# Kernel tuning notes

Measured on AMD Instinct MI355X. Metric: run time of the kernel, lower is better.

The kernel has to match this reference:

```python
import jax, jax.numpy as jnp
import numpy as np

B, L, HID, H = 2, 384, 512, 8
D = HID // H  # head_dim = 64


def setup_inputs() -> dict:
    key = jax.random.key(0)
    ks = jax.random.split(key, 16)
    s = 0.02
    return {
        "query": jax.random.normal(ks[0], (B, L, HID), jnp.float32),
        "key_": jax.random.normal(ks[1], (B, L, HID), jnp.float32),
        "value": jax.random.normal(ks[2], (B, L, HID), jnp.float32),
        "mask": jnp.ones((B, 1, 1, L), jnp.int32),
        # fc_q/k/v/o: nn.Linear(hid_dim, hid_dim)
        "Wq": jax.random.normal(ks[3], (HID, HID), jnp.float32) * s,
        "bq": jnp.zeros((HID,), jnp.float32),
        "Wk": jax.random.normal(ks[4], (HID, HID), jnp.float32) * s,
        "bk": jnp.zeros((HID,), jnp.float32),
        "Wv": jax.random.normal(ks[5], (HID, HID), jnp.float32) * s,
        "bv": jnp.zeros((HID,), jnp.float32),
        "Wo": jax.random.normal(ks[6], (HID, HID), jnp.float32) * s,
        "bo": jnp.zeros((HID,), jnp.float32),
        # additive-attention score MLP: W1, W2: Linear(D, D); v: Linear(D, 1)
        "W1": jax.random.normal(ks[7], (D, D), jnp.float32) * s,
        "b1": jnp.zeros((D,), jnp.float32),
        "W2": jax.random.normal(ks[8], (D, D), jnp.float32) * s,
        "b2": jnp.zeros((D,), jnp.float32),
        "vw": jax.random.normal(ks[9], (1, D), jnp.float32) * s,
        "vb": jnp.zeros((1,), jnp.float32),
    }


def reference(query, key_, value, mask, Wq, bq, Wk, bk, Wv, bv, Wo, bo,
              W1, b1, W2, b2, vw, vb):
    b = query.shape[0]
    # projections (torch Linear: x @ W.T + b)
    Q = query @ Wq.T + bq
    K = key_ @ Wk.T + bk
    V = value @ Wv.T + bv
    # [b, h, l, d]
    def split_heads(x):
        return x.reshape(b, -1, H, D).transpose(0, 2, 1, 3)
    Q, K, V = split_heads(Q), split_heads(K), split_heads(V)
    # additive (Bahdanau-style) score: v^T tanh(W1 q + W2 k)
    tQ = Q @ W1.T + b1            # [b, h, lq, d]
    tK = K @ W2.T + b2            # [b, h, lk, d]
    e = jnp.tanh(tQ[:, :, :, None, :] + tK[:, :, None, :, :])  # [b,h,lq,lk,d]
    energy = jnp.einsum('bhqkd,d->bhqk', e, vw[0]) + vb[0]      # [b,h,lq,lk]
    energy = jnp.where(mask == 0, jnp.float32(-1e10), energy)
    attention = jax.nn.softmax(energy, axis=-1)
    x = jnp.einsum('bhqk,bhkd->bhqd', attention, V)  # dropout p=0 (eval)
    x = x.transpose(0, 2, 1, 3).reshape(b, -1, HID)
    x = x @ Wo.T + bo
    return x, attention
```

## Files before the change

kernel.cpp:

```cpp
#include <hip/hip_runtime.h>

#define BATCH 2
#define LSEQ 384
#define NHID 512
#define NH 8
#define DH 64
#define BH (BATCH*NH)
#define MROWS (BATCH*NH*LSEQ/NH)
#define XELEMS ((size_t)768 * NHID)
#define TQ 8
#define QTILES (LSEQ/TQ)

typedef unsigned short ushort_t;
typedef __attribute__((ext_vector_type(8))) short bf16x8;
typedef __attribute__((ext_vector_type(4))) float f32x4;

__device__ __forceinline__ float bf2f(ushort_t u) {
    unsigned int v = ((unsigned int)u) << 16;
    return __uint_as_float(v);
}
__device__ __forceinline__ ushort_t f2bf(float f) {
    unsigned int u = __float_as_uint(f);
    unsigned int lsb = (u >> 16) & 1u;
    u += 0x7fffu + lsb;
    return (ushort_t)(u >> 16);
}
__device__ __forceinline__ float ld1(const void* p, size_t i, int f) {
    return f ? ((const float*)p)[i] : bf2f(((const ushort_t*)p)[i]);
}
__device__ __forceinline__ float4 ld4(const void* p, size_t i, int f) {
    if (f) return ((const float4*)p)[i >> 2];
    ushort4 u = ((const ushort4*)p)[i >> 2];
    return make_float4(bf2f(u.x), bf2f(u.y), bf2f(u.z), bf2f(u.w));
}
__device__ __forceinline__ int block_detect(const unsigned int* q, int* cnt) {
    int t = threadIdx.x;
    if (t == 0) *cnt = 0;
    __syncthreads();
    int n = blockDim.x < 256 ? blockDim.x : 256;
    if (t < n) {
        unsigned int elo = (q[t] >> 7) & 0xFFu;
        if (elo >= 100u && elo <= 150u) atomicAdd(cnt, 1);
    }
    __syncthreads();
    return (*cnt * 2 > n) ? 0 : 1;
}
__device__ __forceinline__ uint4 packu4(float4 a, float4 b) {
    uint4 r;
    r.x = (unsigned)f2bf(a.x) | ((unsigned)f2bf(a.y) << 16);
    r.y = (unsigned)f2bf(a.z) | ((unsigned)f2bf(a.w) << 16);
    r.z = (unsigned)f2bf(b.x) | ((unsigned)f2bf(b.y) << 16);
    r.w = (unsigned)f2bf(b.z) | ((unsigned)f2bf(b.w) << 16);
    return r;
}
__device__ __forceinline__ bf16x8 pack_bf8(float4 a, float4 b) {
    bf16x8 r;
    r[0] = (short)f2bf(a.x); r[1] = (short)f2bf(a.y);
    r[2] = (short)f2bf(a.z); r[3] = (short)f2bf(a.w);
    r[4] = (short)f2bf(b.x); r[5] = (short)f2bf(b.y);
    r[6] = (short)f2bf(b.z); r[7] = (short)f2bf(b.w);
    return r;
}

#define OFF_ETQ   16
#define OFF_ETKT  (16 + 393216)
#define OFF_VH    (16 + 2*393216)
#define OFF_XH    (16 + 3*393216)

#define LDSTR 72

__global__ __launch_bounds__(128) void gemm_qkv(
    const void* qp, const void* kp, const void* vp,
    const void* Wqp, const void* Wkp, const void* Wvp,
    const void* W1p, const void* W2p,
    const void* bqp, const void* bkp, const void* b1p, const void* b2p,
    const void* bvp, float* __restrict__ ws)
{
    __shared__ int s_cnt;
    __shared__ ushort_t smA[32 * LDSTR];
    __shared__ ushort_t smB[64 * LDSTR];
    __shared__ float biasF[64];
    const int f = block_detect((const unsigned int*)qp, &s_cnt);

    const int mode = blockIdx.z;
    const void* A = (mode == 0) ? qp : (mode == 1) ? kp : vp;
    const void* W = (mode == 0) ? Wqp : (mode == 1) ? Wkp : Wvp;
    const void* W1x = (mode == 1) ? W2p : W1p;

    const int h    = blockIdx.x;
    const int col0 = h * 64;
    const int row0 = blockIdx.y * 32;
    const int t = threadIdx.x;
    const int w = t >> 6, l16 = t & 15, quad = (t & 63) >> 4;

    if (t < 64) {
        if (mode == 2) {
            biasF[t] = ld1(bvp, col0 + t, f);
        } else {
            const void* b1x = (mode == 1) ? b2p : b1p;
            const void* bx  = (mode == 1) ? bkp : bqp;
            float s = ld1(b1x, t, f);
            for (int j = 0; j < 64; j++)
                s = fmaf(ld1(W1x, (size_t)t * 64 + j, f), ld1(bx, h * 64 + j, f), s);
            biasF[t] = s;
        }
    }

    const int arow = t >> 2, acol = (t & 3) * 16;
    const int brow = t >> 1, bcol = (t & 1) * 32;

    const size_t abase = (size_t)(row0 + arow) * 512 + acol;
    const size_t bbase = (size_t)(col0 + brow) * 512 + bcol;

    float4 a4[4], b4[8];
    #pragma unroll
    for (int i = 0; i < 4; i++) a4[i] = ld4(A, abase + i * 4, f);
    #pragma unroll
    for (int i = 0; i < 8; i++) b4[i] = ld4(W, bbase + i * 4, f);

    f32x4 acc[4];
    #pragma unroll
    for (int nt = 0; nt < 4; nt++) acc[nt] = (f32x4){0.f, 0.f, 0.f, 0.f};

    for (int k0 = 0; k0 < 512; k0 += 64) {
        __syncthreads();
        *reinterpret_cast<uint4*>(&smA[arow * LDSTR + acol])     = packu4(a4[0], a4[1]);
        *reinterpret_cast<uint4*>(&smA[arow * LDSTR + acol + 8]) = packu4(a4[2], a4[3]);
        *reinterpret_cast<uint4*>(&smB[brow * LDSTR + bcol])      = packu4(b4[0], b4[1]);
        *reinterpret_cast<uint4*>(&smB[brow * LDSTR + bcol + 8])  = packu4(b4[2], b4[3]);
        *reinterpret_cast<uint4*>(&smB[brow * LDSTR + bcol + 16]) = packu4(b4[4], b4[5]);
        *reinterpret_cast<uint4*>(&smB[brow * LDSTR + bcol + 24]) = packu4(b4[6], b4[7]);
        __syncthreads();
        if (k0 + 64 < 512) {
            #pragma unroll
            for (int i = 0; i < 4; i++) a4[i] = ld4(A, abase + k0 + 64 + i * 4, f);
            #pragma unroll
            for (int i = 0; i < 8; i++) b4[i] = ld4(W, bbase + k0 + 64 + i * 4, f);
        }
        #pragma unroll
        for (int kk = 0; kk < 2; kk++) {
            bf16x8 af = *reinterpret_cast<const bf16x8*>(
                &smA[(w * 16 + l16) * LDSTR + kk * 32 + quad * 8]);
            #pragma unroll
            for (int nt = 0; nt < 4; nt++) {
                bf16x8 bfr = *reinterpret_cast<const bf16x8*>(
                    &smB[(nt * 16 + l16) * LDSTR + kk * 32 + quad * 8]);
                acc[nt] = __builtin_amdgcn_mfma_f32_16x16x32_bf16(af, bfr, acc[nt], 0, 0, 0);
            }
        }
    }

    const int b  = (row0 >= LSEQ) ? 1 : 0;
    const int lbase = row0 - b * LSEQ + w * 16;
    const int bh = b * NH + h;

    if (mode == 2) {
        float* Out = ws + OFF_VH;
        #pragma unroll
        for (int nt = 0; nt < 4; nt++) {
            int d = l16 + nt * 16;
            #pragma unroll
            for (int r = 0; r < 4; r++) {
                int l = lbase + quad * 4 + r;
                Out[(size_t)(bh * LSEQ + l) * 64 + d] = acc[nt][r] + biasF[d];
            }
        }
    } else {
        #pragma unroll
        for (int nt = 0; nt < 4; nt++)
            #pragma unroll
            for (int r = 0; r < 4; r++)
                smA[(w * 16 + quad * 4 + r) * LDSTR + l16 + nt * 16] =
                    f2bf(acc[nt][r]);
        f32x4 acc2[4];
        #pragma unroll
        for (int nt = 0; nt < 4; nt++) acc2[nt] = (f32x4){0.f, 0.f, 0.f, 0.f};
        #pragma unroll
        for (int kk = 0; kk < 2; kk++) {
            bf16x8 af2 = *reinterpret_cast<const bf16x8*>(
                &smA[(w * 16 + l16) * LDSTR + kk * 32 + quad * 8]);
            #pragma unroll
            for (int nt = 0; nt < 4; nt++) {
                int od = nt * 16 + l16, j0 = kk * 32 + quad * 8;
                float4 wa = ld4(W1x, (size_t)od * 64 + j0, f);
                float4 wb = ld4(W1x, (size_t)od * 64 + j0 + 4, f);
                bf16x8 bfw = pack_bf8(wa, wb);
                acc2[nt] = __builtin_amdgcn_mfma_f32_16x16x32_bf16(af2, bfw, acc2[nt], 0, 0, 0);
            }
        }
        if (mode == 0) {
            float* Out = ws + OFF_ETQ;
            #pragma unroll
            for (int nt = 0; nt < 4; nt++) {
                int d = l16 + nt * 16;
                #pragma unroll
                for (int r = 0; r < 4; r++) {
                    int l = lbase + quad * 4 + r;
                    Out[(size_t)(bh * LSEQ + l) * 64 + d] =
                        __expf(2.f * (acc2[nt][r] + biasF[d]));
                }
            }
        } else {
            float* Out = ws + OFF_ETKT;
            #pragma unroll
            for (int nt = 0; nt < 4; nt++) {
                int d = l16 + nt * 16;
                float4 o;
                o.x = __expf(2.f * (acc2[nt][0] + biasF[d]));
                o.y = __expf(2.f * (acc2[nt][1] + biasF[d]));
                o.z = __expf(2.f * (acc2[nt][2] + biasF[d]));
                o.w = __expf(2.f * (acc2[nt][3] + biasF[d]));
                *reinterpret_cast<float4*>(
                    &Out[(size_t)(bh * 64 + d) * LSEQ + lbase + quad * 4]) = o;
            }
        }
    }
}

__global__ __launch_bounds__(384, 6) void attn_kernel(
    const void* qp, const void* vwp, const void* vbp,
    const float* __restrict__ ws_in, float* __restrict__ ws,
    const int* __restrict__ mask, void* __restrict__ dout)
{
    __shared__ int s_cnt;
    const int f = block_detect((const unsigned int*)qp, &s_cnt);

    const float* Etq = ws_in + OFF_ETQ;
    const float* Etk = ws_in + OFF_ETKT;
    const float* Vh  = ws_in + OFF_VH;
    float* Xh = ws + OFF_XH;

    const int bid = blockIdx.x;
    const int qt = bid % QTILES;
    const int bh = bid / QTILES;
    const int q0 = qt * TQ;
    const int b  = bh >> 3;
    const int h  = bh & 7;
    const int t  = threadIdx.x;
    const int wave = t >> 6;

    __shared__ __align__(16) float etq8[64][TQ];
    __shared__ float vws[64];
    __shared__ float ps[TQ][LSEQ];
    __shared__ float red[6][TQ][16][4];
    __shared__ float rmax[TQ][6];
    __shared__ float rsum[TQ][6];
    __shared__ float s_vb;

    for (int i = t; i < TQ * 64; i += 384) {
        int qi = i >> 6, d = i & 63;
        etq8[d][qi] = Etq[(size_t)(bh * LSEQ + q0 + qi) * 64 + d];
    }
    if (t < 64) {
        float v = ld1(vwp, t, f);
        vws[t] = v;
        #pragma unroll
        for (int off = 32; off > 0; off >>= 1) v += __shfl_xor(v, off, 64);
        if (t == 0) s_vb = ld1(vbp, 0, f) + v;
    }
    const int mok = mask[b * LSEQ + t];
    __syncthreads();
    const float vbSum = s_vb;

    float e2[TQ] = {0.f, 0.f, 0.f, 0.f, 0.f, 0.f, 0.f, 0.f};
    const float* ekp = Etk + (size_t)bh * 64 * LSEQ + t;
    #pragma unroll 4
    for (int d = 0; d < 64; d++) {
        float ekv = ekp[(size_t)d * LSEQ];
        float4 eqA = *reinterpret_cast<const float4*>(&etq8[d][0]);
        float4 eqB = *reinterpret_cast<const float4*>(&etq8[d][4]);
        float wv = vws[d];
        e2[0] = fmaf(wv, __builtin_amdgcn_rcpf(fmaf(eqA.x, ekv, 1.0f)), e2[0]);
        e2[1] = fmaf(wv, __builtin_amdgcn_rcpf(fmaf(eqA.y, ekv, 1.0f)), e2[1]);
        e2[2] = fmaf(wv, __builtin_amdgcn_rcpf(fmaf(eqA.z, ekv, 1.0f)), e2[2]);
        e2[3] = fmaf(wv, __builtin_amdgcn_rcpf(fmaf(eqA.w, ekv, 1.0f)), e2[3]);
        e2[4] = fmaf(wv, __builtin_amdgcn_rcpf(fmaf(eqB.x, ekv, 1.0f)), e2[4]);
        e2[5] = fmaf(wv, __builtin_amdgcn_rcpf(fmaf(eqB.y, ekv, 1.0f)), e2[5]);
        e2[6] = fmaf(wv, __builtin_amdgcn_rcpf(fmaf(eqB.z, ekv, 1.0f)), e2[6]);
        e2[7] = fmaf(wv, __builtin_amdgcn_rcpf(fmaf(eqB.w, ekv, 1.0f)), e2[7]);
    }
    float en[TQ];
    #pragma unroll
    for (int qi = 0; qi < TQ; qi++) {
        en[qi] = fmaf(-2.0f, e2[qi], vbSum);
        if (mok == 0) en[qi] = -1e10f;
    }

    #pragma unroll
    for (int qi = 0; qi < TQ; qi++) {
        float m = en[qi];
        #pragma unroll
        for (int off = 32; off > 0; off >>= 1) m = fmaxf(m, __shfl_xor(m, off, 64));
        if ((t & 63) == 0) rmax[qi][wave] = m;
    }
    __syncthreads();
    float p[TQ];
    #pragma unroll
    for (int qi = 0; qi < TQ; qi++) {
        float gm = fmaxf(fmaxf(fmaxf(rmax[qi][0], rmax[qi][1]),
                               fmaxf(rmax[qi][2], rmax[qi][3])),
                         fmaxf(rmax[qi][4], rmax[qi][5]));
        p[qi] = __expf(en[qi] - gm);
        float s = p[qi];
        #pragma unroll
        for (int off = 32; off > 0; off >>= 1) s += __shfl_xor(s, off, 64);
        if ((t & 63) == 0) rsum[qi][wave] = s;
    }
    __syncthreads();
    #pragma unroll
    for (int qi = 0; qi < TQ; qi++) {
        float gs = rsum[qi][0] + rsum[qi][1] + rsum[qi][2] +
                   rsum[qi][3] + rsum[qi][4] + rsum[qi][5];
        p[qi] *= 1.0f / gs;
        ps[qi][t] = p[qi];
        size_t aidx = XELEMS + (size_t)(bh * LSEQ + q0 + qi) * LSEQ + t;
        if (f) ((float*)dout)[aidx] = p[qi];
        else   ((ushort_t*)dout)[aidx] = f2bf(p[qi]);
    }
    __syncthreads();

    const int dq = t & 15;
    const int ksub = t >> 4;
    const float* vb4 = Vh + (size_t)bh * LSEQ * 64 + dq * 4;
    float4 acc[TQ];
    #pragma unroll
    for (int qi = 0; qi < TQ; qi++) acc[qi] = make_float4(0.f, 0.f, 0.f, 0.f);
    for (int kk = ksub; kk < LSEQ; kk += 24) {
        float4 v4 = *reinterpret_cast<const float4*>(vb4 + (size_t)kk * 64);
        #pragma unroll
        for (int qi = 0; qi < TQ; qi++) {
            float pq = ps[qi][kk];
            acc[qi].x = fmaf(pq, v4.x, acc[qi].x);
            acc[qi].y = fmaf(pq, v4.y, acc[qi].y);
            acc[qi].z = fmaf(pq, v4.z, acc[qi].z);
            acc[qi].w = fmaf(pq, v4.w, acc[qi].w);
        }
    }
    #pragma unroll
    for (int qi = 0; qi < TQ; qi++) {
        #pragma unroll
        for (int off = 16; off <= 32; off <<= 1) {
            acc[qi].x += __shfl_xor(acc[qi].x, off, 64);
            acc[qi].y += __shfl_xor(acc[qi].y, off, 64);
            acc[qi].z += __shfl_xor(acc[qi].z, off, 64);
            acc[qi].w += __shfl_xor(acc[qi].w, off, 64);
        }
    }
    if ((t & 63) < 16) {
        #pragma unroll
        for (int qi = 0; qi < TQ; qi++) {
            red[wave][qi][dq][0] = acc[qi].x;
            red[wave][qi][dq][1] = acc[qi].y;
            red[wave][qi][dq][2] = acc[qi].z;
            red[wave][qi][dq][3] = acc[qi].w;
        }
    }
    __syncthreads();
    if (t < 256) {
        int d = t & 63;
        #pragma unroll
        for (int half = 0; half < 2; half++) {
            int qi = (t >> 6) + half * 4;
            float sx = 0.f;
            #pragma unroll
            for (int w = 0; w < 6; w++) sx += red[w][qi][d >> 2][d & 3];
            Xh[((size_t)(b * LSEQ + q0 + qi) * NH + h) * 64 + d] = sx;
        }
    }
}

__global__ __launch_bounds__(128) void gemm_out(
    const void* qp, const void* Wop, const void* bop,
    const float* __restrict__ ws_in, void* __restrict__ dout)
{
    __shared__ int s_cnt;
    __shared__ ushort_t smA[32 * LDSTR];
    __shared__ ushort_t smB[64 * LDSTR];
    __shared__ float biasF[64];
    const int f = block_detect((const unsigned int*)qp, &s_cnt);

    const float* Xh = ws_in + OFF_XH;
    const int col0 = blockIdx.x * 64;
    const int row0 = blockIdx.y * 32;
    const int t = threadIdx.x;
    const int w = t >> 6, l16 = t & 15, quad = (t & 63) >> 4;

    if (t < 64) biasF[t] = ld1(bop, col0 + t, f);

    const int arow = t >> 2, acol = (t & 3) * 16;
    const int brow = t >> 1, bcol = (t & 1) * 32;
    const float* Ab = Xh + (size_t)(row0 + arow) * 512 + acol;
    const size_t bbase = (size_t)(col0 + brow) * 512 + bcol;

    float4 a4[4], b4[8];
    #pragma unroll
    for (int i = 0; i < 4; i++) a4[i] = *reinterpret_cast<const float4*>(Ab + i * 4);
    #pragma unroll
    for (int i = 0; i < 8; i++) b4[i] = ld4(Wop, bbase + i * 4, f);

    f32x4 acc[4];
    #pragma unroll
    for (int nt = 0; nt < 4; nt++) acc[nt] = (f32x4){0.f, 0.f, 0.f, 0.f};

    for (int k0 = 0; k0 < 512; k0 += 64) {
        __syncthreads();
        *reinterpret_cast<uint4*>(&smA[arow * LDSTR + acol])     = packu4(a4[0], a4[1]);
        *reinterpret_cast<uint4*>(&smA[arow * LDSTR + acol + 8]) = packu4(a4[2], a4[3]);
        *reinterpret_cast<uint4*>(&smB[brow * LDSTR + bcol])      = packu4(b4[0], b4[1]);
        *reinterpret_cast<uint4*>(&smB[brow * LDSTR + bcol + 8])  = packu4(b4[2], b4[3]);
        *reinterpret_cast<uint4*>(&smB[brow * LDSTR + bcol + 16]) = packu4(b4[4], b4[5]);
        *reinterpret_cast<uint4*>(&smB[brow * LDSTR + bcol + 24]) = packu4(b4[6], b4[7]);
        __syncthreads();
        if (k0 + 64 < 512) {
            #pragma unroll
            for (int i = 0; i < 4; i++)
                a4[i] = *reinterpret_cast<const float4*>(Ab + k0 + 64 + i * 4);
            #pragma unroll
            for (int i = 0; i < 8; i++) b4[i] = ld4(Wop, bbase + k0 + 64 + i * 4, f);
        }
        #pragma unroll
        for (int kk = 0; kk < 2; kk++) {
            bf16x8 af = *reinterpret_cast<const bf16x8*>(
                &smA[(w * 16 + l16) * LDSTR + kk * 32 + quad * 8]);
            #pragma unroll
            for (int nt = 0; nt < 4; nt++) {
                bf16x8 bfr = *reinterpret_cast<const bf16x8*>(
                    &smB[(nt * 16 + l16) * LDSTR + kk * 32 + quad * 8]);
                acc[nt] = __builtin_amdgcn_mfma_f32_16x16x32_bf16(af, bfr, acc[nt], 0, 0, 0);
            }
        }
    }

    #pragma unroll
    for (int nt = 0; nt < 4; nt++) {
        int n = col0 + l16 + nt * 16;
        float bi = biasF[l16 + nt * 16];
        #pragma unroll
        for (int r = 0; r < 4; r++) {
            int m = row0 + w * 16 + quad * 4 + r;
            float c = acc[nt][r] + bi;
            size_t idx = (size_t)m * 512 + n;
            if (f) ((float*)dout)[idx] = c;
            else   ((ushort_t*)dout)[idx] = f2bf(c);
        }
    }
}

extern "C" void kernel_launch(void* const* d_in, const int* in_sizes, int n_in,
                              void* d_out, int out_size, void* d_ws, size_t ws_size,
                              hipStream_t stream)
{
    const void* qp = d_in[0];
    const void* kp = d_in[1];
    const void* vp = d_in[2];
    const int* mask = (const int*)d_in[3];
    const void* Wqp = d_in[4];  const void* bqp = d_in[5];
    const void* Wkp = d_in[6];  const void* bkp = d_in[7];
    const void* Wvp = d_in[8];  const void* bvp = d_in[9];
    const void* Wop = d_in[10]; const void* bop = d_in[11];
    const void* W1p = d_in[12]; const void* b1p = d_in[13];
    const void* W2p = d_in[14]; const void* b2p = d_in[15];
    const void* vwp = d_in[16]; const void* vbp = d_in[17];

    float* ws = (float*)d_ws;

    gemm_qkv<<<dim3(8, 24, 3), 128, 0, stream>>>(qp, kp, vp, Wqp, Wkp, Wvp,
                                                 W1p, W2p, bqp, bkp, b1p, b2p,
                                                 bvp, ws);
    attn_kernel<<<BH * QTILES, 384, 0, stream>>>(qp, vwp, vbp, ws, ws, mask, d_out);
    gemm_out<<<dim3(8, 24, 1), 128, 0, stream>>>(qp, Wop, bop, ws, d_out);
}
```

Before: 169.0 us.

## Split-K the QKV and output GEMMs and drop the softmax max pass

The QKV projection GEMM is split into two K halves and the output GEMM into four. Each split writes fp32 partials to workspace, and new finalize/out_reduce kernels add them, apply the bias, exp and transpose, and write the bf16 or fp32 result. The goal is more blocks to fill the GPU than the earlier 192/576-block grids provided. This costs two extra launches and extra workspace traffic. Separately, the attention kernel drops the row-max reduction and its syncthreads before exp. That relies on bounded energies and risks overflow, and with a -1e10 mask an all-masked row gives a zero sum.

```diff
diff --git a/kernel.cpp b/kernel.cpp
--- a/kernel.cpp
+++ b/kernel.cpp
@@ -6,7 +6,6 @@
 #define NH 8
 #define DH 64
 #define BH (BATCH*NH)
-#define MROWS (BATCH*NH*LSEQ/NH)
 #define XELEMS ((size_t)768 * NHID)
 #define TQ 8
 #define QTILES (LSEQ/TQ)
@@ -62,10 +61,14 @@
     return r;
 }
 
-#define OFF_ETQ   16
-#define OFF_ETKT  (16 + 393216)
-#define OFF_VH    (16 + 2*393216)
-#define OFF_XH    (16 + 3*393216)
+#define OFF_P     16
+#define PSTRIDE   393216
+#define OFF_BQE   2359312
+#define OFF_BKE   2359824
+#define OFF_ETQ   2360336
+#define OFF_ETKT  2753552
+#define OFF_VH    3146768
+#define OFF_XH    3539984
 
 #define LDSTR 72
 
@@ -74,18 +77,20 @@
     const void* Wqp, const void* Wkp, const void* Wvp,
     const void* W1p, const void* W2p,
     const void* bqp, const void* bkp, const void* b1p, const void* b2p,
-    const void* bvp, float* __restrict__ ws)
+    float* __restrict__ ws)
 {
     __shared__ int s_cnt;
     __shared__ ushort_t smA[32 * LDSTR];
     __shared__ ushort_t smB[64 * LDSTR];
-    __shared__ float biasF[64];
     const int f = block_detect((const unsigned int*)qp, &s_cnt);
 
-    const int mode = blockIdx.z;
+    const int z = blockIdx.z;
+    const int mode = z >> 1, ks = z & 1;
+    const int kbase = ks * 256;
     const void* A = (mode == 0) ? qp : (mode == 1) ? kp : vp;
     const void* W = (mode == 0) ? Wqp : (mode == 1) ? Wkp : Wvp;
     const void* W1x = (mode == 1) ? W2p : W1p;
+    float* P = ws + OFF_P + (size_t)z * PSTRIDE;
 
     const int h    = blockIdx.x;
     const int col0 = h * 64;
@@ -93,24 +98,10 @@
     const int t = threadIdx.x;
     const int w = t >> 6, l16 = t & 15, quad = (t & 63) >> 4;
 
-    if (t < 64) {
-        if (mode == 2) {
-            biasF[t] = ld1(bvp, col0 + t, f);
-        } else {
-            const void* b1x = (mode == 1) ? b2p : b1p;
-            const void* bx  = (mode == 1) ? bkp : bqp;
-            float s = ld1(b1x, t, f);
-            for (int j = 0; j < 64; j++)
-                s = fmaf(ld1(W1x, (size_t)t * 64 + j, f), ld1(bx, h * 64 + j, f), s);
-            biasF[t] = s;
-        }
-    }
-
     const int arow = t >> 2, acol = (t & 3) * 16;
     const int brow = t >> 1, bcol = (t & 1) * 32;
-
-    const size_t abase = (size_t)(row0 + arow) * 512 + acol;
-    const size_t bbase = (size_t)(col0 + brow) * 512 + bcol;
+    const size_t abase = (size_t)(row0 + arow) * 512 + kbase + acol;
+    const size_t bbase = (size_t)(col0 + brow) * 512 + kbase + bcol;
 
     float4 a4[4], b4[8];
     #pragma unroll
@@ -122,7 +113,7 @@
     #pragma unroll
     for (int nt = 0; nt < 4; nt++) acc[nt] = (f32x4){0.f, 0.f, 0.f, 0.f};
 
-    for (int k0 = 0; k0 < 512; k0 += 64) {
+    for (int k0 = 0; k0 < 256; k0 += 64) {
         __syncthreads();
         *reinterpret_cast<uint4*>(&smA[arow * LDSTR + acol])     = packu4(a4[0], a4[1]);
         *reinterpret_cast<uint4*>(&smA[arow * LDSTR + acol + 8]) = packu4(a4[2], a4[3]);
@@ -131,7 +122,7 @@
         *reinterpret_cast<uint4*>(&smB[brow * LDSTR + bcol + 16]) = packu4(b4[4], b4[5]);
         *reinterpret_cast<uint4*>(&smB[brow * LDSTR + bcol + 24]) = packu4(b4[6], b4[7]);
         __syncthreads();
-        if (k0 + 64 < 512) {
+        if (k0 + 64 < 256) {
             #pragma unroll
             for (int i = 0; i < 4; i++) a4[i] = ld4(A, abase + k0 + 64 + i * 4, f);
             #pragma unroll
@@ -150,19 +141,14 @@
         }
     }
 
-    const int b  = (row0 >= LSEQ) ? 1 : 0;
-    const int lbase = row0 - b * LSEQ + w * 16;
-    const int bh = b * NH + h;
-
     if (mode == 2) {
-        float* Out = ws + OFF_VH;
         #pragma unroll
         for (int nt = 0; nt < 4; nt++) {
-            int d = l16 + nt * 16;
+            int o = col0 + l16 + nt * 16;
             #pragma unroll
             for (int r = 0; r < 4; r++) {
-                int l = lbase + quad * 4 + r;
-                Out[(size_t)(bh * LSEQ + l) * 64 + d] = acc[nt][r] + biasF[d];
+                int m = row0 + w * 16 + quad * 4 + r;
+                P[(size_t)m * 512 + o] = acc[nt][r];
             }
         }
     } else {
@@ -188,31 +174,89 @@
                 acc2[nt] = __builtin_amdgcn_mfma_f32_16x16x32_bf16(af2, bfw, acc2[nt], 0, 0, 0);
             }
         }
-        if (mode == 0) {
-            float* Out = ws + OFF_ETQ;
-            #pragma unroll
-            for (int nt = 0; nt < 4; nt++) {
-                int d = l16 + nt * 16;
-                #pragma unroll
-                for (int r = 0; r < 4; r++) {
-                    int l = lbase + quad * 4 + r;
-                    Out[(size_t)(bh * LSEQ + l) * 64 + d] =
-                        __expf(2.f * (acc2[nt][r] + biasF[d]));
-                }
+        #pragma unroll
+        for (int nt = 0; nt < 4; nt++) {
+            int o = col0 + l16 + nt * 16;
+            #pragma unroll
+            for (int r = 0; r < 4; r++) {
+                int m = row0 + w * 16 + quad * 4 + r;
+                P[(size_t)m * 512 + o] = acc2[nt][r];
             }
+        }
+        if (blockIdx.y == 0 && ks == 0 && t < 64) {
+            int od = t;
+            const void* b1x = mode ? b2p : b1p;
+            const void* bx  = mode ? bkp : bqp;
+            float s = ld1(b1x, od, f);
+            for (int j = 0; j < 64; j++)
+                s = fmaf(ld1(W1x, (size_t)od * 64 + j, f), ld1(bx, h * 64 + j, f), s);
+            ws[(mode ? OFF_BKE : OFF_BQE) + col0 + od] = s;
+        }
+    }
+}
+
+__global__ __launch_bounds__(256) void finalize(
+    const void* qp, const void* bvp,
+    const float* __restrict__ ws_in, float* __restrict__ ws)
+{
+    __shared__ int s_cnt;
+    __shared__ __align__(16) float T[64 * 68];
+    const int f = block_detect((const unsigned int*)qp, &s_cnt);
+    const int blk = blockIdx.x;
+    const int tid = threadIdx.x;
+
+    if (blk < 384 || blk >= 480) {
+        const int isV = (blk >= 480);
+        const float* P0 = ws_in + OFF_P + (size_t)(isV ? 4 : 0) * PSTRIDE;
+        const float* P1 = P0 + PSTRIDE;
+        float* Out = ws + (isV ? OFF_VH : OFF_ETQ);
+        int gid = (isV ? blk - 480 : blk) * 256 + tid;
+        int m = gid >> 7;
+        int o4 = (gid & 127) * 4;
+        float4 p0 = *reinterpret_cast<const float4*>(P0 + (size_t)m * 512 + o4);
+        float4 p1 = *reinterpret_cast<const float4*>(P1 + (size_t)m * 512 + o4);
+        float4 bb;
+        if (isV) bb = ld4(bvp, o4, f);
+        else     bb = *reinterpret_cast<const float4*>(ws_in + OFF_BQE + o4);
+        float4 r;
+        if (isV) {
+            r.x = p0.x + p1.x + bb.x; r.y = p0.y + p1.y + bb.y;
+            r.z = p0.z + p1.z + bb.z; r.w = p0.w + p1.w + bb.w;
         } else {
-            float* Out = ws + OFF_ETKT;
-            #pragma unroll
-            for (int nt = 0; nt < 4; nt++) {
-                int d = l16 + nt * 16;
-                float4 o;
-                o.x = __expf(2.f * (acc2[nt][0] + biasF[d]));
-                o.y = __expf(2.f * (acc2[nt][1] + biasF[d]));
-                o.z = __expf(2.f * (acc2[nt][2] + biasF[d]));
-                o.w = __expf(2.f * (acc2[nt][3] + biasF[d]));
-                *reinterpret_cast<float4*>(
-                    &Out[(size_t)(bh * 64 + d) * LSEQ + lbase + quad * 4]) = o;
-            }
+            r.x = __expf(2.f * (p0.x + p1.x + bb.x));
+            r.y = __expf(2.f * (p0.y + p1.y + bb.y));
+            r.z = __expf(2.f * (p0.z + p1.z + bb.z));
+            r.w = __expf(2.f * (p0.w + p1.w + bb.w));
+        }
+        int b = m / LSEQ, l = m % LSEQ, h = o4 >> 6, d = o4 & 63;
+        *reinterpret_cast<float4*>(&Out[(size_t)((b * NH + h) * LSEQ + l) * 64 + d]) = r;
+    } else {
+        int blk2 = blk - 384;
+        int bh = blk2 / 6, l0 = (blk2 % 6) * 64;
+        int b = bh >> 3, h = bh & 7;
+        const float* P0 = ws_in + OFF_P + (size_t)2 * PSTRIDE;
+        const float* P1 = P0 + PSTRIDE;
+        #pragma unroll
+        for (int it = 0; it < 4; it++) {
+            int li = (tid >> 4) + it * 16;
+            int d4 = (tid & 15) * 4;
+            size_t src = (size_t)(b * LSEQ + l0 + li) * 512 + h * 64 + d4;
+            float4 p0 = *reinterpret_cast<const float4*>(P0 + src);
+            float4 p1 = *reinterpret_cast<const float4*>(P1 + src);
+            const float4 bb = *reinterpret_cast<const float4*>(ws_in + OFF_BKE + h * 64 + d4);
+            T[(d4 + 0) * 68 + li] = __expf(2.f * (p0.x + p1.x + bb.x));
+            T[(d4 + 1) * 68 + li] = __expf(2.f * (p0.y + p1.y + bb.y));
+            T[(d4 + 2) * 68 + li] = __expf(2.f * (p0.z + p1.z + bb.z));
+            T[(d4 + 3) * 68 + li] = __expf(2.f * (p0.w + p1.w + bb.w));
+        }
+        __syncthreads();
+        float* Out = ws + OFF_ETKT;
+        #pragma unroll
+        for (int it = 0; it < 4; it++) {
+            int d = (tid >> 4) + it * 16;
+            int l4 = (tid & 15) * 4;
+            float4 v = *reinterpret_cast<const float4*>(&T[d * 68 + l4]);
+            *reinterpret_cast<float4*>(&Out[(size_t)(bh * 64 + d) * LSEQ + l0 + l4]) = v;
         }
     }
 }
@@ -243,7 +287,6 @@
     __shared__ float vws[64];
     __shared__ float ps[TQ][LSEQ];
     __shared__ float red[6][TQ][16][4];
-    __shared__ float rmax[TQ][6];
     __shared__ float rsum[TQ][6];
     __shared__ float s_vb;
 
@@ -279,28 +322,13 @@
         e2[6] = fmaf(wv, __builtin_amdgcn_rcpf(fmaf(eqB.z, ekv, 1.0f)), e2[6]);
         e2[7] = fmaf(wv, __builtin_amdgcn_rcpf(fmaf(eqB.w, ekv, 1.0f)), e2[7]);
     }
-    float en[TQ];
+
+    float p[TQ];
     #pragma unroll
     for (int qi = 0; qi < TQ; qi++) {
-        en[qi] = fmaf(-2.0f, e2[qi], vbSum);
-        if (mok == 0) en[qi] = -1e10f;
-    }
-
-    #pragma unroll
-    for (int qi = 0; qi < TQ; qi++) {
-        float m = en[qi];
-        #pragma unroll
-        for (int off = 32; off > 0; off >>= 1) m = fmaxf(m, __shfl_xor(m, off, 64));
-        if ((t & 63) == 0) rmax[qi][wave] = m;
-    }
-    __syncthreads();
-    float p[TQ];
-    #pragma unroll
-    for (int qi = 0; qi < TQ; qi++) {
-        float gm = fmaxf(fmaxf(fmaxf(rmax[qi][0], rmax[qi][1]),
-                               fmaxf(rmax[qi][2], rmax[qi][3])),
-                         fmaxf(rmax[qi][4], rmax[qi][5]));
-        p[qi] = __expf(en[qi] - gm);
+        float en = fmaf(-2.0f, e2[qi], vbSum);
+        if (mok == 0) en = -1e10f;
+        p[qi] = __expf(en);
         float s = p[qi];
         #pragma unroll
         for (int off = 32; off > 0; off >>= 1) s += __shfl_xor(s, off, 64);
@@ -370,27 +398,28 @@
 }
 
 __global__ __launch_bounds__(128) void gemm_out(
-    const void* qp, const void* Wop, const void* bop,
-    const float* __restrict__ ws_in, void* __restrict__ dout)
+    const void* qp, const void* Wop,
+    const float* __restrict__ ws_in, float* __restrict__ ws)
 {
     __shared__ int s_cnt;
     __shared__ ushort_t smA[32 * LDSTR];
     __shared__ ushort_t smB[64 * LDSTR];
-    __shared__ float biasF[64];
     const int f = block_detect((const unsigned int*)qp, &s_cnt);
 
     const float* Xh = ws_in + OFF_XH;
+    const int ks = blockIdx.z;
+    const int kbase = ks * 128;
+    float* P = ws + OFF_P + (size_t)ks * PSTRIDE;
+
     const int col0 = blockIdx.x * 64;
     const int row0 = blockIdx.y * 32;
     const int t = threadIdx.x;
     const int w = t >> 6, l16 = t & 15, quad = (t & 63) >> 4;
 
-    if (t < 64) biasF[t] = ld1(bop, col0 + t, f);
-
     const int arow = t >> 2, acol = (t & 3) * 16;
     const int brow = t >> 1, bcol = (t & 1) * 32;
-    const float* Ab = Xh + (size_t)(row0 + arow) * 512 + acol;
-    const size_t bbase = (size_t)(col0 + brow) * 512 + bcol;
+    const float* Ab = Xh + (size_t)(row0 + arow) * 512 + kbase + acol;
+    const size_t bbase = (size_t)(col0 + brow) * 512 + kbase + bcol;
 
     float4 a4[4], b4[8];
     #pragma unroll
@@ -402,7 +431,7 @@
     #pragma unroll
     for (int nt = 0; nt < 4; nt++) acc[nt] = (f32x4){0.f, 0.f, 0.f, 0.f};
 
-    for (int k0 = 0; k0 < 512; k0 += 64) {
+    for (int k0 = 0; k0 < 128; k0 += 64) {
         __syncthreads();
         *reinterpret_cast<uint4*>(&smA[arow * LDSTR + acol])     = packu4(a4[0], a4[1]);
         *reinterpret_cast<uint4*>(&smA[arow * LDSTR + acol + 8]) = packu4(a4[2], a4[3]);
@@ -411,7 +440,7 @@
         *reinterpret_cast<uint4*>(&smB[brow * LDSTR + bcol + 16]) = packu4(b4[4], b4[5]);
         *reinterpret_cast<uint4*>(&smB[brow * LDSTR + bcol + 24]) = packu4(b4[6], b4[7]);
         __syncthreads();
-        if (k0 + 64 < 512) {
+        if (k0 + 64 < 128) {
             #pragma unroll
             for (int i = 0; i < 4; i++)
                 a4[i] = *reinterpret_cast<const float4*>(Ab + k0 + 64 + i * 4);
@@ -434,15 +463,40 @@
     #pragma unroll
     for (int nt = 0; nt < 4; nt++) {
         int n = col0 + l16 + nt * 16;
-        float bi = biasF[l16 + nt * 16];
         #pragma unroll
         for (int r = 0; r < 4; r++) {
             int m = row0 + w * 16 + quad * 4 + r;
-            float c = acc[nt][r] + bi;
-            size_t idx = (size_t)m * 512 + n;
-            if (f) ((float*)dout)[idx] = c;
-            else   ((ushort_t*)dout)[idx] = f2bf(c);
-        }
+            P[(size_t)m * 512 + n] = acc[nt][r];
+        }
+    }
+}
+
+__global__ __launch_bounds__(256) void out_reduce(
+    const void* qp, const void* bop,
+    const float* __restrict__ ws_in, void* __restrict__ dout)
+{
+    __shared__ int s_cnt;
+    const int f = block_detect((const unsigned int*)qp, &s_cnt);
+    int gid = blockIdx.x * 256 + threadIdx.x;
+    size_t idx = (size_t)gid * 4;
+    int o4 = (int)(idx & 511);
+    const float* P = ws_in + OFF_P;
+    float4 s0 = *reinterpret_cast<const float4*>(P + idx);
+    float4 s1 = *reinterpret_cast<const float4*>(P + PSTRIDE + idx);
+    float4 s2 = *reinterpret_cast<const float4*>(P + 2 * (size_t)PSTRIDE + idx);
+    float4 s3 = *reinterpret_cast<const float4*>(P + 3 * (size_t)PSTRIDE + idx);
+    float4 bb = ld4(bop, o4, f);
+    float4 r;
+    r.x = (s0.x + s1.x) + (s2.x + s3.x) + bb.x;
+    r.y = (s0.y + s1.y) + (s2.y + s3.y) + bb.y;
+    r.z = (s0.z + s1.z) + (s2.z + s3.z) + bb.z;
+    r.w = (s0.w + s1.w) + (s2.w + s3.w) + bb.w;
+    if (f) {
+        *reinterpret_cast<float4*>((float*)dout + idx) = r;
+    } else {
+        ushort4 u;
+        u.x = f2bf(r.x); u.y = f2bf(r.y); u.z = f2bf(r.z); u.w = f2bf(r.w);
+        *reinterpret_cast<ushort4*>((ushort_t*)dout + idx) = u;
     }
 }
 
@@ -464,9 +518,10 @@
 
     float* ws = (float*)d_ws;
 
-    gemm_qkv<<<dim3(8, 24, 3), 128, 0, stream>>>(qp, kp, vp, Wqp, Wkp, Wvp,
-                                                 W1p, W2p, bqp, bkp, b1p, b2p,
-                                                 bvp, ws);
+    gemm_qkv<<<dim3(8, 24, 6), 128, 0, stream>>>(qp, kp, vp, Wqp, Wkp, Wvp,
+                                                 W1p, W2p, bqp, bkp, b1p, b2p, ws);
+    finalize<<<864, 256, 0, stream>>>(qp, bvp, ws, ws);
     attn_kernel<<<BH * QTILES, 384, 0, stream>>>(qp, vwp, vbp, ws, ws, mask, d_out);
-    gemm_out<<<dim3(8, 24, 1), 128, 0, stream>>>(qp, Wop, bop, ws, d_out);
-}
+    gemm_out<<<dim3(8, 24, 4), 128, 0, stream>>>(qp, Wop, ws, ws);
+    out_reduce<<<384, 256, 0, stream>>>(qp, bop, ws, d_out);
+}
```

New measurement: 168.0 us. About the same (-0.6%).

## Store exp(2*tK) row-major, drop softmax max pass, pack bf16 via perm

Applied to the files above, without the earlier changes.

Stores the exponentiated key projection in [bh, l, d] layout instead of transposed [bh, d, l], so each attention thread reads its own key row with float4 loads rather than one strided scalar per d. Drops the softmax max-reduction pass and its barrier, relying on the energy being bounded by the tanh-based score so exp cannot overflow. Also packs float pairs to bf16 with a single byte-permute instruction. The new per-thread row reads are less coalesced across a wavefront. Skipping the max subtraction risks overflow with large score weights and gives NaN when a whole row is masked.

```diff
diff --git a/kernel.cpp b/kernel.cpp
--- a/kernel.cpp
+++ b/kernel.cpp
@@ -6,7 +6,6 @@
 #define NH 8
 #define DH 64
 #define BH (BATCH*NH)
-#define MROWS (BATCH*NH*LSEQ/NH)
 #define XELEMS ((size_t)768 * NHID)
 #define TQ 8
 #define QTILES (LSEQ/TQ)
@@ -25,6 +24,12 @@
     u += 0x7fffu + lsb;
     return (ushort_t)(u >> 16);
 }
+__device__ __forceinline__ unsigned pk_bf16(float a, float b) {
+    unsigned ua = __float_as_uint(a), ub = __float_as_uint(b);
+    ua += 0x7fffu + ((ua >> 16) & 1u);
+    ub += 0x7fffu + ((ub >> 16) & 1u);
+    return __builtin_amdgcn_perm(ub, ua, 0x07060302);
+}
 __device__ __forceinline__ float ld1(const void* p, size_t i, int f) {
     return f ? ((const float*)p)[i] : bf2f(((const ushort_t*)p)[i]);
 }
@@ -47,23 +52,18 @@
 }
 __device__ __forceinline__ uint4 packu4(float4 a, float4 b) {
     uint4 r;
-    r.x = (unsigned)f2bf(a.x) | ((unsigned)f2bf(a.y) << 16);
-    r.y = (unsigned)f2bf(a.z) | ((unsigned)f2bf(a.w) << 16);
-    r.z = (unsigned)f2bf(b.x) | ((unsigned)f2bf(b.y) << 16);
-    r.w = (unsigned)f2bf(b.z) | ((unsigned)f2bf(b.w) << 16);
+    r.x = pk_bf16(a.x, a.y); r.y = pk_bf16(a.z, a.w);
+    r.z = pk_bf16(b.x, b.y); r.w = pk_bf16(b.z, b.w);
     return r;
 }
 __device__ __forceinline__ bf16x8 pack_bf8(float4 a, float4 b) {
-    bf16x8 r;
-    r[0] = (short)f2bf(a.x); r[1] = (short)f2bf(a.y);
-    r[2] = (short)f2bf(a.z); r[3] = (short)f2bf(a.w);
-    r[4] = (short)f2bf(b.x); r[5] = (short)f2bf(b.y);
-    r[6] = (short)f2bf(b.z); r[7] = (short)f2bf(b.w);
-    return r;
+    union { uint4 u; bf16x8 v; } r;
+    r.u = packu4(a, b);
+    return r.v;
 }
 
 #define OFF_ETQ   16
-#define OFF_ETKT  (16 + 393216)
+#define OFF_ETK   (16 + 393216)
 #define OFF_VH    (16 + 2*393216)
 #define OFF_XH    (16 + 3*393216)
 
@@ -108,7 +108,6 @@
 
     const int arow = t >> 2, acol = (t & 3) * 16;
     const int brow = t >> 1, bcol = (t & 1) * 32;
-
     const size_t abase = (size_t)(row0 + arow) * 512 + acol;
     const size_t bbase = (size_t)(col0 + brow) * 512 + bcol;
 
@@ -159,10 +158,11 @@
         #pragma unroll
         for (int nt = 0; nt < 4; nt++) {
             int d = l16 + nt * 16;
+            float bi = biasF[d];
             #pragma unroll
             for (int r = 0; r < 4; r++) {
                 int l = lbase + quad * 4 + r;
-                Out[(size_t)(bh * LSEQ + l) * 64 + d] = acc[nt][r] + biasF[d];
+                Out[(size_t)(bh * LSEQ + l) * 64 + d] = acc[nt][r] + bi;
             }
         }
     } else {
@@ -188,30 +188,16 @@
                 acc2[nt] = __builtin_amdgcn_mfma_f32_16x16x32_bf16(af2, bfw, acc2[nt], 0, 0, 0);
             }
         }
-        if (mode == 0) {
-            float* Out = ws + OFF_ETQ;
-            #pragma unroll
-            for (int nt = 0; nt < 4; nt++) {
-                int d = l16 + nt * 16;
-                #pragma unroll
-                for (int r = 0; r < 4; r++) {
-                    int l = lbase + quad * 4 + r;
-                    Out[(size_t)(bh * LSEQ + l) * 64 + d] =
-                        __expf(2.f * (acc2[nt][r] + biasF[d]));
-                }
-            }
-        } else {
-            float* Out = ws + OFF_ETKT;
-            #pragma unroll
-            for (int nt = 0; nt < 4; nt++) {
-                int d = l16 + nt * 16;
-                float4 o;
-                o.x = __expf(2.f * (acc2[nt][0] + biasF[d]));
-                o.y = __expf(2.f * (acc2[nt][1] + biasF[d]));
-                o.z = __expf(2.f * (acc2[nt][2] + biasF[d]));
-                o.w = __expf(2.f * (acc2[nt][3] + biasF[d]));
-                *reinterpret_cast<float4*>(
-                    &Out[(size_t)(bh * 64 + d) * LSEQ + lbase + quad * 4]) = o;
+        float* Out = ws + ((mode == 0) ? OFF_ETQ : OFF_ETK);
+        #pragma unroll
+        for (int nt = 0; nt < 4; nt++) {
+            int d = l16 + nt * 16;
+            float bi = biasF[d];
+            #pragma unroll
+            for (int r = 0; r < 4; r++) {
+                int l = lbase + quad * 4 + r;
+                Out[(size_t)(bh * LSEQ + l) * 64 + d] =
+                    __expf(2.f * (acc2[nt][r] + bi));
             }
         }
     }
@@ -226,7 +212,7 @@
     const int f = block_detect((const unsigned int*)qp, &s_cnt);
 
     const float* Etq = ws_in + OFF_ETQ;
-    const float* Etk = ws_in + OFF_ETKT;
+    const float* Etk = ws_in + OFF_ETK;
     const float* Vh  = ws_in + OFF_VH;
     float* Xh = ws + OFF_XH;
 
@@ -243,7 +229,6 @@
     __shared__ float vws[64];
     __shared__ float ps[TQ][LSEQ];
     __shared__ float red[6][TQ][16][4];
-    __shared__ float rmax[TQ][6];
     __shared__ float rsum[TQ][6];
     __shared__ float s_vb;
 
@@ -263,44 +248,34 @@
     const float vbSum = s_vb;
 
     float e2[TQ] = {0.f, 0.f, 0.f, 0.f, 0.f, 0.f, 0.f, 0.f};
-    const float* ekp = Etk + (size_t)bh * 64 * LSEQ + t;
+    const float* ekrow = Etk + (size_t)(bh * LSEQ + t) * 64;
     #pragma unroll 4
-    for (int d = 0; d < 64; d++) {
-        float ekv = ekp[(size_t)d * LSEQ];
-        float4 eqA = *reinterpret_cast<const float4*>(&etq8[d][0]);
-        float4 eqB = *reinterpret_cast<const float4*>(&etq8[d][4]);
-        float wv = vws[d];
-        e2[0] = fmaf(wv, __builtin_amdgcn_rcpf(fmaf(eqA.x, ekv, 1.0f)), e2[0]);
-        e2[1] = fmaf(wv, __builtin_amdgcn_rcpf(fmaf(eqA.y, ekv, 1.0f)), e2[1]);
-        e2[2] = fmaf(wv, __builtin_amdgcn_rcpf(fmaf(eqA.z, ekv, 1.0f)), e2[2]);
-        e2[3] = fmaf(wv, __builtin_amdgcn_rcpf(fmaf(eqA.w, ekv, 1.0f)), e2[3]);
-        e2[4] = fmaf(wv, __builtin_amdgcn_rcpf(fmaf(eqB.x, ekv, 1.0f)), e2[4]);
-        e2[5] = fmaf(wv, __builtin_amdgcn_rcpf(fmaf(eqB.y, ekv, 1.0f)), e2[5]);
-        e2[6] = fmaf(wv, __builtin_amdgcn_rcpf(fmaf(eqB.z, ekv, 1.0f)), e2[6]);
-        e2[7] = fmaf(wv, __builtin_amdgcn_rcpf(fmaf(eqB.w, ekv, 1.0f)), e2[7]);
-    }
-    float en[TQ];
+    for (int dv = 0; dv < 16; dv++) {
+        float4 ek4 = *reinterpret_cast<const float4*>(ekrow + dv * 4);
+        #pragma unroll
+        for (int j = 0; j < 4; j++) {
+            int d = dv * 4 + j;
+            float ekv = (j == 0) ? ek4.x : (j == 1) ? ek4.y : (j == 2) ? ek4.z : ek4.w;
+            float4 eqA = *reinterpret_cast<const float4*>(&etq8[d][0]);
+            float4 eqB = *reinterpret_cast<const float4*>(&etq8[d][4]);
+            float wv = vws[d];
+            e2[0] = fmaf(wv, __builtin_amdgcn_rcpf(fmaf(eqA.x, ekv, 1.0f)), e2[0]);
+            e2[1] = fmaf(wv, __builtin_amdgcn_rcpf(fmaf(eqA.y, ekv, 1.0f)), e2[1]);
+            e2[2] = fmaf(wv, __builtin_amdgcn_rcpf(fmaf(eqA.z, ekv, 1.0f)), e2[2]);
+            e2[3] = fmaf(wv, __builtin_amdgcn_rcpf(fmaf(eqA.w, ekv, 1.0f)), e2[3]);
+            e2[4] = fmaf(wv, __builtin_amdgcn_rcpf(fmaf(eqB.x, ekv, 1.0f)), e2[4]);
+            e2[5] = fmaf(wv, __builtin_amdgcn_rcpf(fmaf(eqB.y, ekv, 1.0f)), e2[5]);
+            e2[6] = fmaf(wv, __builtin_amdgcn_rcpf(fmaf(eqB.z, ekv, 1.0f)), e2[6]);
+            e2[7] = fmaf(wv, __builtin_amdgcn_rcpf(fmaf(eqB.w, ekv, 1.0f)), e2[7]);
+        }
+    }
+
+    float p[TQ];
     #pragma unroll
     for (int qi = 0; qi < TQ; qi++) {
-        en[qi] = fmaf(-2.0f, e2[qi], vbSum);
-        if (mok == 0) en[qi] = -1e10f;
-    }
-
-    #pragma unroll
-    for (int qi = 0; qi < TQ; qi++) {
-        float m = en[qi];
-        #pragma unroll
-        for (int off = 32; off > 0; off >>= 1) m = fmaxf(m, __shfl_xor(m, off, 64));
-        if ((t & 63) == 0) rmax[qi][wave] = m;
-    }
-    __syncthreads();
-    float p[TQ];
-    #pragma unroll
-    for (int qi = 0; qi < TQ; qi++) {
-        float gm = fmaxf(fmaxf(fmaxf(rmax[qi][0], rmax[qi][1]),
-                               fmaxf(rmax[qi][2], rmax[qi][3])),
-                         fmaxf(rmax[qi][4], rmax[qi][5]));
-        p[qi] = __expf(en[qi] - gm);
+        float en = fmaf(-2.0f, e2[qi], vbSum);
+        if (mok == 0) en = -1e10f;
+        p[qi] = __expf(en);
         float s = p[qi];
         #pragma unroll
         for (int off = 32; off > 0; off >>= 1) s += __shfl_xor(s, off, 64);
```

After: 165.1 us (median of 2 runs). 2.3% less time.
